# Optimization experiments

Measured on AMD Instinct MI355X. Metric: run time of the kernel, lower is better.

## Reference

```python
import jax, jax.numpy as jnp
import numpy as np

N_GRID = 64          # voxels per side (must be 2**i)
SIDE = 2.0           # cube side length, centered at origin (0,0,0)
N1 = N_GRID + 1      # grid points per side
B = 262144           # number of query points
W_FEAT = 256         # feature channels per grid point


def setup_inputs() -> dict:
    key = jax.random.key(0)
    k1, k2, k3 = jax.random.split(key, 3)
    x = jax.random.uniform(k1, (B, 3), minval=-1.0, maxval=1.0, dtype=jnp.float32)
    grid_value = jax.random.normal(k2, (N1 ** 3, 1), dtype=jnp.float32)
    grid_feature = jax.random.normal(k3, (N1 ** 3, W_FEAT), dtype=jnp.float32)
    return {"x": x, "grid_value": grid_value, "grid_feature": grid_feature}


def _trilinear(x, grid_value, grid_feature):
    # Map points into voxel coordinates. Volume is [-SIDE/2, SIDE/2]^3.
    min_c = -SIDE / 2.0
    rel = (x - min_c) * (N_GRID / SIDE)             # (B,3) in [0, N_GRID] if inside
    valid = jnp.all((rel >= 0.0) & (rel <= float(N_GRID)), axis=-1)  # (B,)
    idx = jnp.clip(jnp.floor(rel).astype(jnp.int32), 0, N_GRID - 1)  # (B,3) voxel idx
    t = rel - idx.astype(rel.dtype)                 # (B,3) fractional offset in voxel
    base = (idx[:, 0] * N1 + idx[:, 1]) * N1 + idx[:, 2]            # flat grid-pt idx

    out = jnp.zeros((x.shape[0], 1), x.dtype)
    feat = jnp.zeros((x.shape[0], grid_feature.shape[1]), x.dtype)
    # Fixed 8-corner loop (structural, not over data dims): trilinear gather + weighted sum.
    for ox in (0, 1):
        wx = t[:, 0] if ox else 1.0 - t[:, 0]
        for oy in (0, 1):
            wy = t[:, 1] if oy else 1.0 - t[:, 1]
            for oz in (0, 1):
                wz = t[:, 2] if oz else 1.0 - t[:, 2]
                w = (wx * wy * wz)[:, None]          # (B,1)
                flat = base + (ox * N1 + oy) * N1 + oz
                out = out + w * grid_value[flat]
                feat = feat + w * grid_feature[flat]
    m = valid[:, None]
    # Points outside the volume get 0 (matches out[valid_idx] = ... on a zero tensor).
    return jnp.where(m, out, 0.0), jnp.where(m, feat, 0.0)


def reference(x, grid_value, grid_feature):
    return _trilinear(x, grid_value, grid_feature)
```

## Files before the change

### kernel.cpp

```cpp
#include <hip/hip_runtime.h>

#define NG   64
#define N1i  65
#define BPTS 262144
#define NBUCK 4096

__device__ __forceinline__ int point_bucket(const float* __restrict__ x, int p) {
    const float rx = (x[3 * p + 0] + 1.0f) * 32.0f;
    const float ry = (x[3 * p + 1] + 1.0f) * 32.0f;
    const float rz = (x[3 * p + 2] + 1.0f) * 32.0f;
    int ix = min(max((int)floorf(rx), 0), NG - 1) >> 2;
    int iy = min(max((int)floorf(ry), 0), NG - 1) >> 2;
    int iz = min(max((int)floorf(rz), 0), NG - 1) >> 2;
    return (ix * 16 + iy) * 16 + iz;
}

__global__ __launch_bounds__(256) void hist_kernel(
    const float* __restrict__ x, int* __restrict__ counts)
{
    const int p = blockIdx.x * 256 + threadIdx.x;
    atomicAdd(&counts[point_bucket(x, p)], 1);
}

__global__ __launch_bounds__(1024) void scan_kernel(
    const int* __restrict__ counts, int* __restrict__ offsets)
{
    __shared__ int sm[1024];
    const int t = threadIdx.x;
    const int c0 = counts[t * 4 + 0], c1 = counts[t * 4 + 1];
    const int c2 = counts[t * 4 + 2], c3 = counts[t * 4 + 3];
    const int s = c0 + c1 + c2 + c3;
    sm[t] = s;
    __syncthreads();
    int val = s;
    for (int off = 1; off < 1024; off <<= 1) {
        const int v = (t >= off) ? sm[t - off] : 0;
        __syncthreads();
        val += v;
        sm[t] = val;
        __syncthreads();
    }
    const int base = val - s;
    offsets[t * 4 + 0] = base;
    offsets[t * 4 + 1] = base + c0;
    offsets[t * 4 + 2] = base + c0 + c1;
    offsets[t * 4 + 3] = base + c0 + c1 + c2;
}

__global__ __launch_bounds__(256) void scatter_kernel(
    const float* __restrict__ x, int* __restrict__ offsets, int* __restrict__ perm)
{
    const int p = blockIdx.x * 256 + threadIdx.x;
    const int pos = atomicAdd(&offsets[point_bucket(x, p)], 1);
    perm[pos] = p;
}

__global__ __launch_bounds__(256) void trilerp_kernel(
    const float*  __restrict__ x,
    const float*  __restrict__ gv,
    const float4* __restrict__ gf,
    const int*    __restrict__ perm,
    float*        __restrict__ outv,
    float4*       __restrict__ outf)
{
    const int lane = threadIdx.x & 63;
    const int slot = blockIdx.x * 4 + (threadIdx.x >> 6);
    const int p    = perm[slot];

    const float px = x[3 * p + 0];
    const float py = x[3 * p + 1];
    const float pz = x[3 * p + 2];

    const float rx = (px + 1.0f) * 32.0f;
    const float ry = (py + 1.0f) * 32.0f;
    const float rz = (pz + 1.0f) * 32.0f;

    const bool valid = (rx >= 0.0f) & (rx <= 64.0f) &
                       (ry >= 0.0f) & (ry <= 64.0f) &
                       (rz >= 0.0f) & (rz <= 64.0f);

    int ix = (int)floorf(rx); ix = min(max(ix, 0), NG - 1);
    int iy = (int)floorf(ry); iy = min(max(iy, 0), NG - 1);
    int iz = (int)floorf(rz); iz = min(max(iz, 0), NG - 1);

    const float tx = rx - (float)ix;
    const float ty = ry - (float)iy;
    const float tz = rz - (float)iz;

    const int base = (ix * N1i + iy) * N1i + iz;

    const float wx0 = 1.0f - tx, wy0 = 1.0f - ty, wz0 = 1.0f - tz;
    float w[8];
    w[0] = wx0 * wy0 * wz0;
    w[1] = wx0 * wy0 * tz;
    w[2] = wx0 * ty  * wz0;
    w[3] = wx0 * ty  * tz;
    w[4] = tx  * wy0 * wz0;
    w[5] = tx  * wy0 * tz;
    w[6] = tx  * ty  * wz0;
    w[7] = tx  * ty  * tz;

    const int off[8] = {0, 1, N1i, N1i + 1,
                        N1i * N1i, N1i * N1i + 1, N1i * N1i + N1i, N1i * N1i + N1i + 1};

    float4 acc = make_float4(0.f, 0.f, 0.f, 0.f);
#pragma unroll
    for (int c = 0; c < 8; ++c) {
        const float4 v = gf[(size_t)(base + off[c]) * 64 + lane];
        acc.x += w[c] * v.x;
        acc.y += w[c] * v.y;
        acc.z += w[c] * v.z;
        acc.w += w[c] * v.w;
    }
    if (!valid) acc = make_float4(0.f, 0.f, 0.f, 0.f);
    outf[(size_t)p * 64 + lane] = acc;

    if (lane == 0) {
        float s = 0.0f;
#pragma unroll
        for (int c = 0; c < 8; ++c) s += w[c] * gv[base + off[c]];
        outv[p] = valid ? s : 0.0f;
    }
}

extern "C" void kernel_launch(void* const* d_in, const int* in_sizes, int n_in,
                              void* d_out, int out_size, void* d_ws, size_t ws_size,
                              hipStream_t stream) {
    const float*  x  = (const float*)d_in[0];
    const float*  gv = (const float*)d_in[1];
    const float4* gf = (const float4*)d_in[2];

    float*  outv = (float*)d_out;
    float4* outf = (float4*)((float*)d_out + BPTS);

    int* counts  = (int*)d_ws;
    int* offsets = counts + NBUCK;
    int* perm    = offsets + NBUCK;

    hipMemsetAsync(counts, 0, NBUCK * sizeof(int), stream);
    hist_kernel   <<<BPTS / 256, 256,  0, stream>>>(x, counts);
    scan_kernel   <<<1,          1024, 0, stream>>>(counts, offsets);
    scatter_kernel<<<BPTS / 256, 256,  0, stream>>>(x, offsets, perm);
    trilerp_kernel<<<BPTS / 4,   256,  0, stream>>>(x, gv, gf, perm, outv, outf);
}
```

Measured before the change: 615.7 us.

## Morton-order buckets, pad atomic counters, swizzle blocks, nontemporal output stores

Bucket ids are now computed in Morton (Z-order) over 4x4x4 voxel blocks, so consecutively processed points stay spatially close and share gathered grid features in cache. Counters and offsets are interleaved in one table padded to 64-byte stride, which cuts atomic contention on shared cache lines. Trilerp blocks are swizzled across 8 strided groups, likely to spread neighbouring work across XCDs/L2s, and output stores become nontemporal so they do not evict grid data from cache. The swizzle may instead break locality if consecutive blocks were already sharing cache.

```diff
diff --git a/kernel.cpp b/kernel.cpp
--- a/kernel.cpp
+++ b/kernel.cpp
@@ -1,9 +1,12 @@
 #include <hip/hip_runtime.h>
 
-#define NG   64
-#define N1i  65
-#define BPTS 262144
+#define NG    64
+#define N1i   65
+#define BPTS  262144
 #define NBUCK 4096
+#define CPAD  16
+
+typedef float v4f __attribute__((ext_vector_type(4)));
 
 __device__ __forceinline__ int point_bucket(const float* __restrict__ x, int p) {
     const float rx = (x[3 * p + 0] + 1.0f) * 32.0f;
@@ -12,23 +15,29 @@
     int ix = min(max((int)floorf(rx), 0), NG - 1) >> 2;
     int iy = min(max((int)floorf(ry), 0), NG - 1) >> 2;
     int iz = min(max((int)floorf(rz), 0), NG - 1) >> 2;
-    return (ix * 16 + iy) * 16 + iz;
+    int m = 0;
+#pragma unroll
+    for (int i = 0; i < 4; ++i) {
+        m |= ((ix >> i) & 1) << (3 * i + 2);
+        m |= ((iy >> i) & 1) << (3 * i + 1);
+        m |= ((iz >> i) & 1) << (3 * i + 0);
+    }
+    return m;
 }
 
 __global__ __launch_bounds__(256) void hist_kernel(
-    const float* __restrict__ x, int* __restrict__ counts)
+    const float* __restrict__ x, int* __restrict__ table)
 {
     const int p = blockIdx.x * 256 + threadIdx.x;
-    atomicAdd(&counts[point_bucket(x, p)], 1);
+    atomicAdd(&table[point_bucket(x, p) * CPAD], 1);
 }
 
-__global__ __launch_bounds__(1024) void scan_kernel(
-    const int* __restrict__ counts, int* __restrict__ offsets)
+__global__ __launch_bounds__(1024) void scan_kernel(int* __restrict__ table)
 {
     __shared__ int sm[1024];
     const int t = threadIdx.x;
-    const int c0 = counts[t * 4 + 0], c1 = counts[t * 4 + 1];
-    const int c2 = counts[t * 4 + 2], c3 = counts[t * 4 + 3];
+    const int c0 = table[(t * 4 + 0) * CPAD], c1 = table[(t * 4 + 1) * CPAD];
+    const int c2 = table[(t * 4 + 2) * CPAD], c3 = table[(t * 4 + 3) * CPAD];
     const int s = c0 + c1 + c2 + c3;
     sm[t] = s;
     __syncthreads();
@@ -41,17 +50,17 @@
         __syncthreads();
     }
     const int base = val - s;
-    offsets[t * 4 + 0] = base;
-    offsets[t * 4 + 1] = base + c0;
-    offsets[t * 4 + 2] = base + c0 + c1;
-    offsets[t * 4 + 3] = base + c0 + c1 + c2;
+    table[(t * 4 + 0) * CPAD + 1] = base;
+    table[(t * 4 + 1) * CPAD + 1] = base + c0;
+    table[(t * 4 + 2) * CPAD + 1] = base + c0 + c1;
+    table[(t * 4 + 3) * CPAD + 1] = base + c0 + c1 + c2;
 }
 
 __global__ __launch_bounds__(256) void scatter_kernel(
-    const float* __restrict__ x, int* __restrict__ offsets, int* __restrict__ perm)
+    const float* __restrict__ x, int* __restrict__ table, int* __restrict__ perm)
 {
     const int p = blockIdx.x * 256 + threadIdx.x;
-    const int pos = atomicAdd(&offsets[point_bucket(x, p)], 1);
+    const int pos = atomicAdd(&table[point_bucket(x, p) * CPAD + 1], 1);
     perm[pos] = p;
 }
 
@@ -64,7 +73,9 @@
     float4*       __restrict__ outf)
 {
     const int lane = threadIdx.x & 63;
-    const int slot = blockIdx.x * 4 + (threadIdx.x >> 6);
+    const int bid  = blockIdx.x;
+    const int swz  = (bid & 7) * (BPTS / 4 / 8) + (bid >> 3);
+    const int slot = swz * 4 + (threadIdx.x >> 6);
     const int p    = perm[slot];
 
     const float px = x[3 * p + 0];
@@ -113,13 +124,14 @@
         acc.w += w[c] * v.w;
     }
     if (!valid) acc = make_float4(0.f, 0.f, 0.f, 0.f);
-    outf[(size_t)p * 64 + lane] = acc;
+    v4f av = {acc.x, acc.y, acc.z, acc.w};
+    __builtin_nontemporal_store(av, (v4f*)&outf[(size_t)p * 64 + lane]);
 
     if (lane == 0) {
         float s = 0.0f;
 #pragma unroll
         for (int c = 0; c < 8; ++c) s += w[c] * gv[base + off[c]];
-        outv[p] = valid ? s : 0.0f;
+        __builtin_nontemporal_store(valid ? s : 0.0f, &outv[p]);
     }
 }
 
@@ -133,13 +145,12 @@
     float*  outv = (float*)d_out;
     float4* outf = (float4*)((float*)d_out + BPTS);
 
-    int* counts  = (int*)d_ws;
-    int* offsets = counts + NBUCK;
-    int* perm    = offsets + NBUCK;
+    int* table = (int*)d_ws;
+    int* perm  = table + NBUCK * CPAD;
 
-    hipMemsetAsync(counts, 0, NBUCK * sizeof(int), stream);
-    hist_kernel   <<<BPTS / 256, 256,  0, stream>>>(x, counts);
-    scan_kernel   <<<1,          1024, 0, stream>>>(counts, offsets);
-    scatter_kernel<<<BPTS / 256, 256,  0, stream>>>(x, offsets, perm);
+    hipMemsetAsync(table, 0, NBUCK * CPAD * sizeof(int), stream);
+    hist_kernel   <<<BPTS / 256, 256,  0, stream>>>(x, table);
+    scan_kernel   <<<1,          1024, 0, stream>>>(table);
+    scatter_kernel<<<BPTS / 256, 256,  0, stream>>>(x, table, perm);
     trilerp_kernel<<<BPTS / 4,   256,  0, stream>>>(x, gv, gf, perm, outv, outf);
 }
```

Result: faster. 584.9 us (-5.0%).
